# Kernel optimization log

Measured on AMD Instinct MI355X. Metric: run time of the kernel, lower is better.

Reference implementation:

```python
import jax, jax.numpy as jnp
import numpy as np


def setup_inputs() -> dict:
    key = jax.random.key(0)
    k1, k2, k3 = jax.random.split(key, 3)
    B, L, D = 32, 1024, 512
    NN = 512  # 2 * nn_dim
    i = jax.random.normal(k1, (B, L, D), dtype=jnp.float32)
    j = jax.random.normal(k2, (B, L, D), dtype=jnp.float32)
    W_agg = jax.random.normal(k3, (D, NN), dtype=jnp.float32) * (1.0 / np.sqrt(D))
    b_agg = jnp.zeros((NN,), dtype=jnp.float32)
    return {"i": i, "j": j, "W_agg": W_agg, "b_agg": b_agg}


def reference(i, j, W_agg, b_agg):
    # weight[b,l,m] = <i[b,l], j[b,m]>  -- shared score matrix, reused twice
    weight = jnp.einsum('bld,bmd->blm', i, j)
    weight_i = jax.nn.softmax(weight, axis=-1)  # softmax over Lj (keras default last axis)
    weight_j = jax.nn.softmax(weight, axis=1)   # softmax over Li (get_softmax_row, axis=1)
    # weighted_i = dot([weight_i, i], axes=1): contract Li -> [B, Lj, D]
    weighted_i = jnp.einsum('blm,bld->bmd', weight_i, i)
    # weighted_j = dot([weight_j, j], axes=[2,1]): contract Lj -> [B, Li, D]
    weighted_j = jnp.einsum('blm,bmd->bld', weight_j, j)
    output_i = i - weighted_j  # [B, Li, D]
    output_j = j - weighted_i  # [B, Lj, D]
    # agg_nn: shared aggregation net reducing seq dim to 2*nn_dim
    def agg(x):
        return jax.nn.relu(x.mean(axis=1) @ W_agg + b_agg)
    oi = agg(output_i)  # [B, 2*nn_dim]
    oj = agg(output_j)
    # stack on axis=1 then mean over that axis == elementwise average
    return 0.5 * (oi + oj)
```

## Files before the change

### kernel.cpp

```cpp
#include <hip/hip_runtime.h>


#define BB 32
#define LL 1024
#define DD 512
#define NNN 512
#define SPLIT 16
#define ROWS (LL / SPLIT)
#define NVEC (ROWS * DD / 4)
#define T1 1024
#define NWIN (NVEC / T1)

typedef float f4 __attribute__((ext_vector_type(4)));

__global__ __launch_bounds__(T1, 4) void bialign_stage1(
    const float* __restrict__ gi, const float* __restrict__ gj,
    float* __restrict__ part) {
    const int blk = blockIdx.x;
    const int b = blk >> 4;
    const int s = blk & (SPLIT - 1);
    const size_t base = (size_t)b * LL * DD + (size_t)s * ROWS * DD;
    const f4* i4 = (const f4*)(gi + base);
    const f4* j4 = (const f4*)(gj + base);
    const int t = threadIdx.x;

    f4 a[NWIN], c[NWIN];
    #pragma unroll
    for (int w = 0; w < NWIN; ++w) {
        a[w] = __builtin_nontemporal_load(i4 + (size_t)w * T1 + t);
        c[w] = __builtin_nontemporal_load(j4 + (size_t)w * T1 + t);
    }

    f4 acc0 = 0.f, acc1 = 0.f, acc2 = 0.f, acc3 = 0.f;
    #pragma unroll
    for (int w = 0; w < NWIN; w += 4) {
        acc0 += a[w + 0] - c[w + 0];
        acc1 += a[w + 1] - c[w + 1];
        acc2 += a[w + 2] - c[w + 2];
        acc3 += a[w + 3] - c[w + 3];
    }
    acc0 += acc1;
    acc2 += acc3;
    acc0 += acc2;

    __shared__ float sm[8 * DD];
    f4* sm4 = (f4*)sm;
    sm4[(t >> 7) * 128 + (t & 127)] = acc0;
    __syncthreads();
    if (t < 128) {
        f4 s0 = sm4[t];
        #pragma unroll
        for (int g = 1; g < 8; ++g) {
            s0 += sm4[g * 128 + t];
        }
        ((f4*)(part + (size_t)blk * DD))[t] = s0;
    }
}

__global__ __launch_bounds__(256) void bialign_stage2(
    const float* __restrict__ part, const float* __restrict__ W,
    const float* __restrict__ bias, float* __restrict__ out) {
    const int b = blockIdx.x;
    const int ns = blockIdx.y;
    const int t = threadIdx.x;

    __shared__ float u[DD];
    __shared__ float psum[256];
    for (int d = t; d < DD; d += 256) {
        const float* p = part + (size_t)b * SPLIT * DD + d;
        float sum = 0.f;
        #pragma unroll
        for (int k = 0; k < SPLIT; ++k) sum += p[(size_t)k * DD];
        u[d] = sum * (1.0f / (float)LL);
    }
    __syncthreads();

    const int col = ns * 128 + (t & 127);
    const int d0 = (t >> 7) * 256;
    float acc = 0.f;
    #pragma unroll 8
    for (int d = 0; d < 256; ++d) {
        acc = fmaf(u[d0 + d], W[(size_t)(d0 + d) * NNN + col], acc);
    }
    psum[t] = acc;
    __syncthreads();
    if (t < 128) {
        const float dot = psum[t] + psum[t + 128];
        const float bb = bias[col];
        const float r = 0.5f * (fmaxf(dot + bb, 0.f) + fmaxf(bb - dot, 0.f));
        out[(size_t)b * NNN + col] = r;
    }
}

extern "C" void kernel_launch(void* const* d_in, const int* in_sizes, int n_in,
                              void* d_out, int out_size, void* d_ws, size_t ws_size,
                              hipStream_t stream) {
    const float* gi   = (const float*)d_in[0];
    const float* gj   = (const float*)d_in[1];
    const float* W    = (const float*)d_in[2];
    const float* bias = (const float*)d_in[3];
    float* out = (float*)d_out;
    float* part = (float*)d_ws;

    bialign_stage1<<<BB * SPLIT, T1, 0, stream>>>(gi, gj, part);
    bialign_stage2<<<dim3(BB, 4), 256, 0, stream>>>(part, W, bias, out);
}
```

Before: 155.5 us.

## Stream stage-1 loads through LDS with per-wave double-buffered global_load_lds

Stage 1 now copies each window of i and j straight into LDS with global_load_lds, using a two-slot buffer per wave. Hand-coded vmcnt waits keep two windows in flight instead of loading all sixteen vectors into registers up front. The aim is to cut register pressure, and the min-blocks launch bound is dropped. The cost is fewer outstanding memory requests per thread, which may lower achieved bandwidth on this memory-bound reduction. There is also a small risk of a race when a slot's LDS read is followed closely by the next asynchronous write into it.

```diff
diff --git a/kernel.cpp b/kernel.cpp
--- a/kernel.cpp
+++ b/kernel.cpp
@@ -7,15 +7,24 @@
 #define NNN 512
 #define SPLIT 16
 #define ROWS (LL / SPLIT)
-#define NVEC (ROWS * DD / 4)
+#define NF4 (ROWS * DD / 4)
 #define T1 1024
-#define NWIN (NVEC / T1)
+#define NWIN 8
 
 typedef float f4 __attribute__((ext_vector_type(4)));
 
-__global__ __launch_bounds__(T1, 4) void bialign_stage1(
+__device__ __forceinline__ void gl_lds16(const void* g, void* l) {
+    __builtin_amdgcn_global_load_lds(
+        (const __attribute__((address_space(1))) void*)g,
+        (__attribute__((address_space(3))) void*)l, 16, 0, 0);
+}
+
+__global__ __launch_bounds__(T1) void bialign_stage1(
     const float* __restrict__ gi, const float* __restrict__ gj,
     float* __restrict__ part) {
+    __shared__ f4 lds4[4096];
+    char* lds = (char*)lds4;
+
     const int blk = blockIdx.x;
     const int b = blk >> 4;
     const int s = blk & (SPLIT - 1);
@@ -23,36 +32,43 @@
     const f4* i4 = (const f4*)(gi + base);
     const f4* j4 = (const f4*)(gj + base);
     const int t = threadIdx.x;
+    const int wv = t >> 6;
+    const int lane = t & 63;
 
-    f4 a[NWIN], c[NWIN];
+    char* wbase = lds + wv * 4096;
+
+    #define ISSUE(w, p)                                                  \
+        do {                                                             \
+            const int gidx = (w) * T1 + wv * 64 + lane;                  \
+            gl_lds16(i4 + gidx, wbase + (p) * 2048);                     \
+            gl_lds16(j4 + gidx, wbase + (p) * 2048 + 1024);              \
+        } while (0)
+
+    ISSUE(0, 0);
+    ISSUE(1, 1);
+
+    f4 acc0 = 0.f, acc1 = 0.f;
     #pragma unroll
     for (int w = 0; w < NWIN; ++w) {
-        a[w] = __builtin_nontemporal_load(i4 + (size_t)w * T1 + t);
-        c[w] = __builtin_nontemporal_load(j4 + (size_t)w * T1 + t);
-    }
-
-    f4 acc0 = 0.f, acc1 = 0.f, acc2 = 0.f, acc3 = 0.f;
-    #pragma unroll
-    for (int w = 0; w < NWIN; w += 4) {
-        acc0 += a[w + 0] - c[w + 0];
-        acc1 += a[w + 1] - c[w + 1];
-        acc2 += a[w + 2] - c[w + 2];
-        acc3 += a[w + 3] - c[w + 3];
+        if (w == NWIN - 1) __builtin_amdgcn_s_waitcnt(0x0F70);
+        else               __builtin_amdgcn_s_waitcnt(0x0F72);
+        const int p = w & 1;
+        f4 av = *(const f4*)(wbase + p * 2048 + lane * 16);
+        f4 cv = *(const f4*)(wbase + p * 2048 + 1024 + lane * 16);
+        if (w & 1) acc1 += av - cv; else acc0 += av - cv;
+        if (w < NWIN - 2) ISSUE(w + 2, p);
     }
     acc0 += acc1;
-    acc2 += acc3;
-    acc0 += acc2;
+    #undef ISSUE
 
-    __shared__ float sm[8 * DD];
-    f4* sm4 = (f4*)sm;
-    sm4[(t >> 7) * 128 + (t & 127)] = acc0;
+    __syncthreads();
+    f4* sm4 = lds4;
+    sm4[t] = acc0;
     __syncthreads();
     if (t < 128) {
         f4 s0 = sm4[t];
         #pragma unroll
-        for (int g = 1; g < 8; ++g) {
-            s0 += sm4[g * 128 + t];
-        }
+        for (int g = 1; g < 8; ++g) s0 += sm4[g * 128 + t];
         ((f4*)(part + (size_t)blk * DD))[t] = s0;
     }
 }
```

After: 168.7 us. +8.5%, slower.
